# Kernel optimization log

Hardware: AMD Instinct MI355X
Metric: run time of the kernel (lower is better)

The kernel has to match this reference:

```python
import jax, jax.numpy as jnp
import numpy as np

DIM = 1024
N_HEADS = 16
HEAD_DIM = DIM // N_HEADS
MAX_SEQ = 2048
BATCH = 4
SEQ = 2048


def _rope_tables(seq_len, head_dim):
    inv_freq = 1.0 / (10000.0 ** (jnp.arange(0, head_dim, 2, dtype=jnp.float32) / head_dim))
    t = jnp.arange(seq_len, dtype=jnp.float32)
    freqs = jnp.outer(t, inv_freq)            # [S, D/2]
    emb = jnp.concatenate([freqs, freqs], axis=-1)  # [S, D]
    return jnp.cos(emb), jnp.sin(emb)


def setup_inputs() -> dict:
    key = jax.random.key(0)
    kx, kq, kk, kv, ko = jax.random.split(key, 5)
    s = 1.0 / np.sqrt(DIM)
    x = jax.random.normal(kx, (BATCH, SEQ, DIM), dtype=jnp.float32)
    Wq = jax.random.normal(kq, (DIM, DIM), dtype=jnp.float32) * s
    Wk = jax.random.normal(kk, (DIM, DIM), dtype=jnp.float32) * s
    Wv = jax.random.normal(kv, (DIM, DIM), dtype=jnp.float32) * s
    Wo = jax.random.normal(ko, (DIM, DIM), dtype=jnp.float32) * s
    cos, sin = _rope_tables(SEQ, HEAD_DIM)
    mask = jnp.tril(jnp.ones((SEQ, SEQ), dtype=bool))[None, None]  # [1,1,S,S] causal
    return {"x": x, "Wq": Wq, "Wk": Wk, "Wv": Wv, "Wo": Wo,
            "cos": cos, "sin": sin, "mask": mask}


def _rotate_half(t):
    t1, t2 = jnp.split(t, 2, axis=-1)
    return jnp.concatenate([-t2, t1], axis=-1)


def reference(x, Wq, Wk, Wv, Wo, cos, sin, mask):
    B, S, _ = x.shape
    # projections (torch Linear: y = x @ W.T)
    q = (x @ Wq.T).reshape(B, S, N_HEADS, HEAD_DIM)
    k = (x @ Wk.T).reshape(B, S, N_HEADS, HEAD_DIM)
    v = (x @ Wv.T).reshape(B, S, N_HEADS, HEAD_DIM)
    # RoPE on [B,S,H,D]: cos/sin broadcast over batch and heads
    c = cos[None, :S, None, :]
    s_ = sin[None, :S, None, :]
    q = q * c + _rotate_half(q) * s_
    k = k * c + _rotate_half(k) * s_
    # attention, heads-major
    scale = HEAD_DIM ** -0.5
    attn = jnp.einsum('bqhd,bkhd->bhqk', q, k) * scale
    attn = jnp.where(mask, attn, -jnp.inf)
    attn = jax.nn.softmax(attn, axis=-1)
    out = jnp.einsum('bhqk,bkhd->bqhd', attn, v).reshape(B, S, DIM)
    return out @ Wo.T
```

## Files before the change

### kernel.cpp

```cpp
#include <hip/hip_runtime.h>
#include <hip/hip_bf16.h>
#include <stdint.h>

typedef __bf16 bf16;
typedef __bf16 bf16x4 __attribute__((ext_vector_type(4)));
typedef __bf16 bf16x8 __attribute__((ext_vector_type(8)));
typedef float f32x4 __attribute__((ext_vector_type(4)));

static constexpr int DIMM  = 1024;
static constexpr int NHEADS = 16;
static constexpr int HDIM  = 64;
static constexpr int SEQL  = 2048;
static constexpr int NB    = 4;
static constexpr int MTOT  = NB * SEQL;
static constexpr float LOG2E = 1.4426950408889634f;

__device__ __forceinline__ bool probe_fp32(const void* cosT) {
    return *(const uint32_t*)cosT != 0x3F803F80u;
}

__device__ __forceinline__ bf16x8 load8_any(const void* p, size_t off, bool f32) {
    if (f32) {
        const float* q = (const float*)p + off;
        f32x4 a = *(const f32x4*)q;
        f32x4 b = *(const f32x4*)(q + 4);
        bf16x8 r;
        r[0] = (bf16)a[0]; r[1] = (bf16)a[1]; r[2] = (bf16)a[2]; r[3] = (bf16)a[3];
        r[4] = (bf16)b[0]; r[5] = (bf16)b[1]; r[6] = (bf16)b[2]; r[7] = (bf16)b[3];
        return r;
    }
    return *(const bf16x8*)((const bf16*)p + off);
}

__device__ __forceinline__ float loadf_any(const void* p, size_t off, bool f32) {
    return f32 ? ((const float*)p)[off] : (float)((const bf16*)p)[off];
}

__device__ __forceinline__ int swz(int row, int kc) {
    return row * 128 + ((kc ^ (row & 7)) << 4);
}

__device__ __forceinline__ void gl_lds16(const bf16* g, bf16* l) {
    __builtin_amdgcn_global_load_lds(
        (const __attribute__((address_space(1))) unsigned int*)g,
        (__attribute__((address_space(3))) unsigned int*)l,
        16, 0, 0);
}

__global__ __launch_bounds__(256)
void cvt_kernel(const void* __restrict__ x,  const void* __restrict__ Wq,
                const void* __restrict__ Wk, const void* __restrict__ Wv,
                const void* __restrict__ Wo, const void* __restrict__ cosT,
                bf16* __restrict__ xb,  bf16* __restrict__ Wqb,
                bf16* __restrict__ Wkb, bf16* __restrict__ Wvb,
                bf16* __restrict__ Wob)
{
    const bool f32 = probe_fp32(cosT);
    const size_t NX = (size_t)MTOT * DIMM;
    const size_t NW = (size_t)DIMM * DIMM;
    size_t i = ((size_t)blockIdx.x * 256 + threadIdx.x) * 8;
    const void* src; bf16* dst; size_t off;
    if (i < NX) { src = x; dst = xb; off = i; }
    else {
        size_t j = i - NX;
        int wsel = (int)(j >> 20);
        off = j & (NW - 1);
        if      (wsel == 0) { src = Wq; dst = Wqb; }
        else if (wsel == 1) { src = Wk; dst = Wkb; }
        else if (wsel == 2) { src = Wv; dst = Wvb; }
        else                { src = Wo; dst = Wob; }
    }
    *(bf16x8*)(dst + off) = load8_any(src, off, f32);
}

template <class AAddr, class BAddr>
__device__ __forceinline__ void gemm_tile_gl(AAddr ga, BAddr gb,
                                             bf16* As, bf16* Bs, f32x4 acc[4][4])
{
    const int tid  = threadIdx.x;
    const int lane = tid & 63;
    const int w    = tid >> 6;
    const int l15  = lane & 15;
    const int lg   = lane >> 4;
    const int r8   = lane >> 3;
    const int c8   = lane & 7;
    const int wm   = (w >> 1) * 64;
    const int wn   = (w & 1) * 64;

    #pragma unroll
    for (int mf = 0; mf < 4; ++mf)
        #pragma unroll
        for (int nf = 0; nf < 4; ++nf)
            acc[mf][nf] = f32x4{0.f, 0.f, 0.f, 0.f};

    for (int kt = 0; kt < DIMM / 64; ++kt) {
        const int k0 = kt * 64;
        #pragma unroll
        for (int i = 0; i < 4; ++i) {
            const int c   = w * 4 + i;
            const int row = c * 8 + r8;
            gl_lds16(ga(row, k0 + c8 * 8), As + c * 512);
            gl_lds16(gb(row, k0 + c8 * 8), Bs + c * 512);
        }
        __syncthreads();
        #pragma unroll
        for (int ks = 0; ks < 2; ++ks) {
            bf16x8 af[4], bfr[4];
            #pragma unroll
            for (int mf = 0; mf < 4; ++mf)
                af[mf] = *(const bf16x8*)(As + (wm + mf * 16 + l15) * 64 + (ks * 4 + lg) * 8);
            #pragma unroll
            for (int nf = 0; nf < 4; ++nf)
                bfr[nf] = *(const bf16x8*)(Bs + (wn + nf * 16 + l15) * 64 + (ks * 4 + lg) * 8);
            #pragma unroll
            for (int mf = 0; mf < 4; ++mf)
                #pragma unroll
                for (int nf = 0; nf < 4; ++nf)
                    acc[mf][nf] = __builtin_amdgcn_mfma_f32_16x16x32_bf16(
                        af[mf], bfr[nf], acc[mf][nf], 0, 0, 0);
        }
        __syncthreads();
    }
}

__global__ __launch_bounds__(256, 2)
void qkv_kernel(const bf16* __restrict__ xb,
                const bf16* __restrict__ Wqb, const bf16* __restrict__ Wkb,
                const bf16* __restrict__ Wvb,
                const void* __restrict__ cosT, const void* __restrict__ sinT,
                bf16* __restrict__ qb, bf16* __restrict__ kb, bf16* __restrict__ vTb)
{
    __shared__ __align__(16) bf16 As[128 * 64];
    __shared__ __align__(16) bf16 Bs[3][128 * 64];

    const bool f32 = probe_fp32(cosT);
    const int bm = (int)blockIdx.x * 128;
    const int bn = (int)blockIdx.y * 128;

    const int tid  = threadIdx.x;
    const int lane = tid & 63;
    const int w    = tid >> 6;
    const int l15  = lane & 15;
    const int lg   = lane >> 4;
    const int r8   = lane >> 3;
    const int c8   = lane & 7;
    const int wm   = (w >> 1) * 64;
    const int wn   = (w & 1) * 64;

    f32x4 acc[3][4][4];
    #pragma unroll
    for (int w3 = 0; w3 < 3; ++w3)
        #pragma unroll
        for (int mf = 0; mf < 4; ++mf)
            #pragma unroll
            for (int nf = 0; nf < 4; ++nf)
                acc[w3][mf][nf] = f32x4{0.f, 0.f, 0.f, 0.f};

    const int kcs = (c8 ^ r8) * 8;

    for (int kt = 0; kt < DIMM / 64; ++kt) {
        const int k0 = kt * 64;
        #pragma unroll
        for (int i = 0; i < 4; ++i) {
            const int c   = w * 4 + i;
            const int row = c * 8 + r8;
            gl_lds16(xb  + (size_t)(bm + row) * DIMM + k0 + kcs, As    + c * 512);
            gl_lds16(Wqb + (size_t)(bn + row) * DIMM + k0 + kcs, Bs[0] + c * 512);
            gl_lds16(Wkb + (size_t)(bn + row) * DIMM + k0 + kcs, Bs[1] + c * 512);
            gl_lds16(Wvb + (size_t)(bn + row) * DIMM + k0 + kcs, Bs[2] + c * 512);
        }
        __syncthreads();
        #pragma unroll
        for (int ks = 0; ks < 2; ++ks) {
            bf16x8 af[4];
            #pragma unroll
            for (int mf = 0; mf < 4; ++mf)
                af[mf] = *(const bf16x8*)((const char*)As + swz(wm + mf * 16 + l15, ks * 4 + lg));
            #pragma unroll
            for (int w3 = 0; w3 < 3; ++w3) {
                bf16x8 bfr[4];
                #pragma unroll
                for (int nf = 0; nf < 4; ++nf)
                    bfr[nf] = *(const bf16x8*)((const char*)Bs[w3] + swz(wn + nf * 16 + l15, ks * 4 + lg));
                #pragma unroll
                for (int mf = 0; mf < 4; ++mf)
                    #pragma unroll
                    for (int nf = 0; nf < 4; ++nf)
                        acc[w3][mf][nf] = __builtin_amdgcn_mfma_f32_16x16x32_bf16(
                            af[mf], bfr[nf], acc[w3][mf][nf], 0, 0, 0);
            }
        }
        __syncthreads();
    }

    #pragma unroll
    for (int mf = 0; mf < 4; ++mf) {
        #pragma unroll
        for (int nf = 0; nf < 4; ++nf) {
            int n = bn + wn + nf * 16 + l15;
            int h = n >> 6;
            int d = n & 63;
            float sign = (d < 32) ? -1.f : 1.f;
            #pragma unroll
            for (int r = 0; r < 4; ++r) {
                int m = bm + wm + mf * 16 + lg * 4 + r;
                int b = m >> 11, s = m & 2047;
                float c  = loadf_any(cosT, s * 64 + d, f32);
                float sv = loadf_any(sinT, s * 64 + d, f32);
                size_t o_qk = ((size_t)((b * NHEADS + h) * SEQL + s)) * HDIM + d;
                float q0 = acc[0][mf][nf][r], q1 = acc[0][mf][nf ^ 2][r];
                float k0v = acc[1][mf][nf][r], k1 = acc[1][mf][nf ^ 2][r];
                qb[o_qk] = (bf16)((q0 * c + sign * q1 * sv) * (0.125f * LOG2E));
                kb[o_qk] = (bf16)(k0v * c + sign * k1 * sv);
                vTb[((size_t)((b * NHEADS + h) * HDIM + d)) * SEQL + s] = (bf16)acc[2][mf][nf][r];
            }
        }
    }
}

__global__ __launch_bounds__(256, 3)
void attn_kernel(bf16* __restrict__ qb, const bf16* __restrict__ kb,
                 const bf16* __restrict__ vTb)
{
    __shared__ __align__(16) bf16 Ks[2][64 * 64];
    __shared__ __align__(16) bf16 Vs[2][64 * 64];
    __shared__ __align__(16) bf16 Pl[4][32 * 64];

    const int bh  = blockIdx.x;
    const int qt  = 15 - (int)blockIdx.y;
    const int tid = threadIdx.x;
    const int lane = tid & 63, w = tid >> 6;
    const int l15 = lane & 15, lg = lane >> 4;

    bf16*       Qp = qb  + (size_t)bh * SEQL * HDIM;
    const bf16* Kp = kb  + (size_t)bh * SEQL * HDIM;
    const bf16* Vp = vTb + (size_t)bh * HDIM * SEQL;

    const int q0  = qt * 128 + w * 32;
    const int njt = 2 * qt + 2;

    bf16x8 qf[2][2];
    #pragma unroll
    for (int mf = 0; mf < 2; ++mf)
        #pragma unroll
        for (int ks = 0; ks < 2; ++ks)
            qf[mf][ks] = *(const bf16x8*)(Qp + (size_t)(q0 + mf * 16 + l15) * HDIM + ks * 32 + lg * 8);

    f32x4 oacc[4][2];
    float lsum[2] = {0.f, 0.f};
    #pragma unroll
    for (int nd = 0; nd < 4; ++nd)
        #pragma unroll
        for (int mf = 0; mf < 2; ++mf)
            oacc[nd][mf] = f32x4{0.f, 0.f, 0.f, 0.f};

    char* Pw = (char*)Pl[w];
    const int l7 = l15 & 7;
    const int srow0 = tid >> 3;
    const int skc   = tid & 7;

    bf16x8 kr[2], vr[2];
    auto issue = [&](int j) {
        const int kk0 = j * 64;
        #pragma unroll
        for (int c = 0; c < 2; ++c) {
            int row = c * 32 + srow0;
            kr[c] = *(const bf16x8*)(Kp + (size_t)(kk0 + row) * HDIM + skc * 8);
            vr[c] = *(const bf16x8*)(Vp + (size_t)row * SEQL + kk0 + skc * 8);
        }
    };
    auto commit = [&](int b) {
        #pragma unroll
        for (int c = 0; c < 2; ++c) {
            int row = c * 32 + srow0;
            *(bf16x8*)((char*)Ks[b] + swz(row, skc)) = kr[c];
            *(bf16x8*)((char*)Vs[b] + swz(row, skc)) = vr[c];
        }
    };

    issue(0);
    commit(0);
    __syncthreads();

    for (int j = 0; j < njt; ++j) {
        const int kk0 = j * 64;
        const int buf = j & 1;
        const bool more = (j + 1 < njt);
        if (more) issue(j + 1);

        f32x4 sacc[4][2];
        #pragma unroll
        for (int nf = 0; nf < 4; ++nf)
            #pragma unroll
            for (int mf = 0; mf < 2; ++mf)
                sacc[nf][mf] = f32x4{0.f, 0.f, 0.f, 0.f};
        #pragma unroll
        for (int ks = 0; ks < 2; ++ks) {
            bf16x8 kf[4];
            #pragma unroll
            for (int nf = 0; nf < 4; ++nf)
                kf[nf] = *(const bf16x8*)((const char*)Ks[buf] + swz(nf * 16 + l15, ks * 4 + lg));
            #pragma unroll
            for (int nf = 0; nf < 4; ++nf)
                #pragma unroll
                for (int mf = 0; mf < 2; ++mf)
                    sacc[nf][mf] = __builtin_amdgcn_mfma_f32_16x16x32_bf16(
                        kf[nf], qf[mf][ks], sacc[nf][mf], 0, 0, 0);
        }

        const bool nm = (kk0 + 63 > q0);
        #pragma unroll
        for (int nf = 0; nf < 4; ++nf) {
            #pragma unroll
            for (int mf = 0; mf < 2; ++mf) {
                float pv[4];
                #pragma unroll
                for (int r = 0; r < 4; ++r) {
                    float s = sacc[nf][mf][r];
                    if (nm) {
                        int kv = kk0 + nf * 16 + lg * 4 + r;
                        int qq = q0 + mf * 16 + l15;
                        if (kv > qq) s = -1.0e30f;
                    }
                    pv[r] = exp2f(s);
                }
                lsum[mf] += (pv[0] + pv[1]) + (pv[2] + pv[3]);
                bf16x4 pb;
                pb[0] = (bf16)pv[0]; pb[1] = (bf16)pv[1];
                pb[2] = (bf16)pv[2]; pb[3] = (bf16)pv[3];
                *(bf16x4*)(Pw + (mf * 16 + l15) * 128
                              + (((2 * nf + (lg >> 1)) ^ l7) << 4) + (lg & 1) * 8) = pb;
            }
        }

        #pragma unroll
        for (int ks = 0; ks < 2; ++ks) {
            bf16x8 pf[2], vf[4];
            #pragma unroll
            for (int mf = 0; mf < 2; ++mf)
                pf[mf] = *(const bf16x8*)(Pw + (mf * 16 + l15) * 128
                                             + (((ks * 4 + lg) ^ l7) << 4));
            #pragma unroll
            for (int nd = 0; nd < 4; ++nd)
                vf[nd] = *(const bf16x8*)((const char*)Vs[buf] + swz(nd * 16 + l15, ks * 4 + lg));
            #pragma unroll
            for (int nd = 0; nd < 4; ++nd)
                #pragma unroll
                for (int mf = 0; mf < 2; ++mf)
                    oacc[nd][mf] = __builtin_amdgcn_mfma_f32_16x16x32_bf16(
                        vf[nd], pf[mf], oacc[nd][mf], 0, 0, 0);
        }

        if (more) {
            commit(buf ^ 1);
            __syncthreads();
        }
    }

    #pragma unroll
    for (int mf = 0; mf < 2; ++mf) {
        lsum[mf] += __shfl_xor(lsum[mf], 16);
        lsum[mf] += __shfl_xor(lsum[mf], 32);
    }
    float inv[2] = {1.f / lsum[0], 1.f / lsum[1]};
    #pragma unroll
    for (int nd = 0; nd < 4; ++nd)
        #pragma unroll
        for (int mf = 0; mf < 2; ++mf) {
            bf16x4 o4;
            #pragma unroll
            for (int r = 0; r < 4; ++r)
                o4[r] = (bf16)(oacc[nd][mf][r] * inv[mf]);
            int s = q0 + mf * 16 + l15;
            int d = nd * 16 + lg * 4;
            *(bf16x4*)(Qp + (size_t)s * HDIM + d) = o4;
        }
}

__global__ __launch_bounds__(256)
void oproj_kernel(const bf16* __restrict__ O, const bf16* __restrict__ Wob,
                  const void* __restrict__ cosT, void* __restrict__ outp)
{
    __shared__ __align__(16) bf16 As[128 * 64];
    __shared__ __align__(16) bf16 Bs[128 * 64];
    const bool f32 = probe_fp32(cosT);
    const int bm = blockIdx.x * 128;
    const int bn = blockIdx.y * 128;

    f32x4 acc[4][4];
    gemm_tile_gl(
        [&](int row, int k) {
            int m = bm + row;
            int b = m >> 11, s = m & 2047;
            int h = k >> 6, dd = k & 63;
            return O + ((size_t)((b * NHEADS + h) * SEQL + s)) * HDIM + dd;
        },
        [&](int row, int k) { return Wob + (size_t)(bn + row) * DIMM + k; },
        As, Bs, acc);

    const int tid = threadIdx.x;
    const int lane = tid & 63, wid = tid >> 6;
    const int l15 = lane & 15, lg = lane >> 4;
    const int wm = (wid >> 1) * 64, wn = (wid & 1) * 64;

    #pragma unroll
    for (int mf = 0; mf < 4; ++mf)
        #pragma unroll
        for (int nf = 0; nf < 4; ++nf) {
            int n = bn + wn + nf * 16 + l15;
            #pragma unroll
            for (int r = 0; r < 4; ++r) {
                int m = bm + wm + mf * 16 + lg * 4 + r;
                float v = acc[mf][nf][r];
                if (f32) ((float*)outp)[(size_t)m * DIMM + n] = v;
                else     ((bf16*)outp)[(size_t)m * DIMM + n] = (bf16)v;
            }
        }
}

extern "C" void kernel_launch(void* const* d_in, const int* in_sizes, int n_in,
                              void* d_out, int out_size, void* d_ws, size_t ws_size,
                              hipStream_t stream)
{
    const void* x    = d_in[0];
    const void* Wq   = d_in[1];
    const void* Wk   = d_in[2];
    const void* Wv   = d_in[3];
    const void* Wo   = d_in[4];
    const void* cosT = d_in[5];
    const void* sinT = d_in[6];

    const size_t NELEM = (size_t)MTOT * DIMM;
    const size_t NW    = (size_t)DIMM * DIMM;
    bf16* qb  = (bf16*)d_ws;
    bf16* kb  = qb + NELEM;
    bf16* vT  = kb + NELEM;
    bf16* xb  = vT + NELEM;
    bf16* Wqb = xb + NELEM;
    bf16* Wkb = Wqb + NW;
    bf16* Wvb = Wkb + NW;
    bf16* Wob = Wvb + NW;

    dim3 blk(256);
    cvt_kernel<<<dim3(6144), blk, 0, stream>>>(x, Wq, Wk, Wv, Wo, cosT,
                                               xb, Wqb, Wkb, Wvb, Wob);

    dim3 g1(MTOT / 128, DIMM / 128);
    qkv_kernel<<<g1, blk, 0, stream>>>(xb, Wqb, Wkb, Wvb, cosT, sinT, qb, kb, vT);

    dim3 g2(NB * NHEADS, SEQL / 128);
    attn_kernel<<<g2, blk, 0, stream>>>(qb, kb, vT);

    dim3 g3(MTOT / 128, DIMM / 128);
    oproj_kernel<<<g3, blk, 0, stream>>>(qb, Wob, cosT, d_out);
}
```

Measured before the change: 183.4 us.

## Double-buffer QKV projection LDS tiles with K=32 stages and async prefetch

New measurement: 174.5 us. 1.05x faster.

```diff
diff --git a/kernel.cpp b/kernel.cpp
--- a/kernel.cpp
+++ b/kernel.cpp
@@ -130,8 +130,10 @@
                 const void* __restrict__ cosT, const void* __restrict__ sinT,
                 bf16* __restrict__ qb, bf16* __restrict__ kb, bf16* __restrict__ vTb)
 {
-    __shared__ __align__(16) bf16 As[128 * 64];
-    __shared__ __align__(16) bf16 Bs[3][128 * 64];
+    __shared__ __align__(16) bf16 As[2][128 * 32];
+    __shared__ __align__(16) bf16 Bq[2][128 * 32];
+    __shared__ __align__(16) bf16 Bk[2][128 * 32];
+    __shared__ __align__(16) bf16 Bv[2][128 * 32];
 
     const bool f32 = probe_fp32(cosT);
     const int bm = (int)blockIdx.x * 128;
@@ -142,8 +144,6 @@
     const int w    = tid >> 6;
     const int l15  = lane & 15;
     const int lg   = lane >> 4;
-    const int r8   = lane >> 3;
-    const int c8   = lane & 7;
     const int wm   = (w >> 1) * 64;
     const int wn   = (w & 1) * 64;
 
@@ -156,42 +156,67 @@
             for (int nf = 0; nf < 4; ++nf)
                 acc[w3][mf][nf] = f32x4{0.f, 0.f, 0.f, 0.f};
 
-    const int kcs = (c8 ^ r8) * 8;
-
-    for (int kt = 0; kt < DIMM / 64; ++kt) {
-        const int k0 = kt * 64;
-        #pragma unroll
-        for (int i = 0; i < 4; ++i) {
-            const int c   = w * 4 + i;
-            const int row = c * 8 + r8;
-            gl_lds16(xb  + (size_t)(bm + row) * DIMM + k0 + kcs, As    + c * 512);
-            gl_lds16(Wqb + (size_t)(bn + row) * DIMM + k0 + kcs, Bs[0] + c * 512);
-            gl_lds16(Wkb + (size_t)(bn + row) * DIMM + k0 + kcs, Bs[1] + c * 512);
-            gl_lds16(Wvb + (size_t)(bn + row) * DIMM + k0 + kcs, Bs[2] + c * 512);
-        }
-        __syncthreads();
-        #pragma unroll
-        for (int ks = 0; ks < 2; ++ks) {
-            bf16x8 af[4];
+    const int c0  = w * 2;
+    const int rp0 = lane >> 3;
+    const int tt  = (lane & 7) ^ rp0;
+    const int rgo = (tt >> 2) << 6;
+    const int kq  = (tt & 3) * 8;
+
+    auto stage = [&](int t, int buf) {
+        const int k0 = t * 32;
+        #pragma unroll
+        for (int i = 0; i < 2; ++i) {
+            const int c  = c0 + i;
+            const int rg = c * 8 + rp0 + rgo;
+            const size_t am = (size_t)(bm + rg) * DIMM + k0 + kq;
+            const size_t an = (size_t)(bn + rg) * DIMM + k0 + kq;
+            gl_lds16(xb  + am, &As[buf][c * 512]);
+            gl_lds16(Wqb + an, &Bq[buf][c * 512]);
+            gl_lds16(Wkb + an, &Bk[buf][c * 512]);
+            gl_lds16(Wvb + an, &Bv[buf][c * 512]);
+        }
+    };
+
+    auto rd = [&](const bf16* base, int row) {
+        return *(const bf16x8*)((const char*)base +
+            (row & 63) * 128 + (((((row >> 6) << 2) | lg) ^ (row & 7)) << 4));
+    };
+
+    auto compute = [&](int buf) {
+        bf16x8 af[4];
+        #pragma unroll
+        for (int mf = 0; mf < 4; ++mf)
+            af[mf] = rd(As[buf], wm + mf * 16 + l15);
+        const bf16* bsel[3] = {Bq[buf], Bk[buf], Bv[buf]};
+        #pragma unroll
+        for (int w3 = 0; w3 < 3; ++w3) {
+            bf16x8 bfr[4];
+            #pragma unroll
+            for (int nf = 0; nf < 4; ++nf)
+                bfr[nf] = rd(bsel[w3], wn + nf * 16 + l15);
             #pragma unroll
             for (int mf = 0; mf < 4; ++mf)
-                af[mf] = *(const bf16x8*)((const char*)As + swz(wm + mf * 16 + l15, ks * 4 + lg));
-            #pragma unroll
-            for (int w3 = 0; w3 < 3; ++w3) {
-                bf16x8 bfr[4];
                 #pragma unroll
                 for (int nf = 0; nf < 4; ++nf)
-                    bfr[nf] = *(const bf16x8*)((const char*)Bs[w3] + swz(wn + nf * 16 + l15, ks * 4 + lg));
-                #pragma unroll
-                for (int mf = 0; mf < 4; ++mf)
-                    #pragma unroll
-                    for (int nf = 0; nf < 4; ++nf)
-                        acc[w3][mf][nf] = __builtin_amdgcn_mfma_f32_16x16x32_bf16(
-                            af[mf], bfr[nf], acc[w3][mf][nf], 0, 0, 0);
-            }
-        }
-        __syncthreads();
-    }
+                    acc[w3][mf][nf] = __builtin_amdgcn_mfma_f32_16x16x32_bf16(
+                        af[mf], bfr[nf], acc[w3][mf][nf], 0, 0, 0);
+        }
+    };
+
+    stage(0, 0);
+    for (int t = 0; t < 31; ++t) {
+        stage(t + 1, (t + 1) & 1);
+        asm volatile("s_waitcnt vmcnt(8)" ::: "memory");
+        __builtin_amdgcn_s_barrier();
+        __builtin_amdgcn_sched_barrier(0);
+        compute(t & 1);
+        __builtin_amdgcn_sched_barrier(0);
+        __builtin_amdgcn_s_barrier();
+    }
+    asm volatile("s_waitcnt vmcnt(0)" ::: "memory");
+    __builtin_amdgcn_s_barrier();
+    __builtin_amdgcn_sched_barrier(0);
+    compute(1);
 
     #pragma unroll
     for (int mf = 0; mf < 4; ++mf) {
```
